# Performance work log

Hardware: AMD Instinct MI355X
Metric: run time of the kernel (lower is better)

Reference implementation:

```python
import jax, jax.numpy as jnp
import numpy as np

B, N_KV, N_Q = 32, 4096, 8
D_INP, D_SLOT, HEADS, MLP_H = 256, 256, 4, 1024
ITERS = 3
EPS = 1e-8


def _ln(x, g, b, eps=1e-5):
    m = jnp.mean(x, axis=-1, keepdims=True)
    v = jnp.var(x, axis=-1, keepdims=True)
    return (x - m) * jax.lax.rsqrt(v + eps) * g + b


def setup_inputs() -> dict:
    key = jax.random.key(0)
    ks = jax.random.split(key, 12)
    def w(k, shape, fan_in):
        return jax.random.normal(k, shape, jnp.float32) / np.float32(np.sqrt(fan_in))
    return {
        "inputs": jax.random.normal(ks[0], (B, N_KV, D_INP), jnp.float32),
        "slots": jax.random.normal(ks[1], (B, N_Q, D_SLOT), jnp.float32),
        "ln_in_g": jnp.ones((D_INP,), jnp.float32), "ln_in_b": jnp.zeros((D_INP,), jnp.float32),
        "ln_slot_g": jnp.ones((D_SLOT,), jnp.float32), "ln_slot_b": jnp.zeros((D_SLOT,), jnp.float32),
        "ln_mlp_g": jnp.ones((D_SLOT,), jnp.float32), "ln_mlp_b": jnp.zeros((D_SLOT,), jnp.float32),
        "Wq": w(ks[2], (D_SLOT, D_SLOT), D_SLOT),
        "Wk": w(ks[3], (D_SLOT, D_INP), D_INP),
        "Wv": w(ks[4], (D_SLOT, D_INP), D_INP),
        "W_ih": w(ks[5], (3 * D_SLOT, D_SLOT), D_SLOT),
        "W_hh": w(ks[6], (3 * D_SLOT, D_SLOT), D_SLOT),
        "b_ih": jnp.zeros((3 * D_SLOT,), jnp.float32),
        "b_hh": jnp.zeros((3 * D_SLOT,), jnp.float32),
        "W1": w(ks[7], (MLP_H, D_SLOT), D_SLOT), "b1": jnp.zeros((MLP_H,), jnp.float32),
        "W2": w(ks[8], (D_SLOT, MLP_H), MLP_H), "b2": jnp.zeros((D_SLOT,), jnp.float32),
    }


def reference(inputs, slots, ln_in_g, ln_in_b, ln_slot_g, ln_slot_b, ln_mlp_g, ln_mlp_b,
              Wq, Wk, Wv, W_ih, W_hh, b_ih, b_hh, W1, b1, W2, b2):
    Bb, Nkv, _ = inputs.shape
    _, Nq, Ds = slots.shape
    hd = Ds // HEADS

    x = _ln(inputs, ln_in_g, ln_in_b)
    # k, v: [B, H, N_kv, hd]; k pre-scaled by hd**-0.5 as in the original
    k = (x @ Wk.T).reshape(Bb, Nkv, HEADS, hd).transpose(0, 2, 1, 3) * (hd ** -0.5)
    v = (x @ Wv.T).reshape(Bb, Nkv, HEADS, hd).transpose(0, 2, 1, 3)

    attn_vis = attn_temp = None
    for it in range(ITERS):
        if it == ITERS - 1:
            slots = jax.lax.stop_gradient(slots)
        slots_prev = slots
        s = _ln(slots, ln_slot_g, ln_slot_b)
        q = (s @ Wq.T).reshape(Bb, Nq, HEADS, hd).transpose(0, 2, 1, 3)  # [B,H,Nq,hd]
        logits = jnp.einsum('bhnd,bhqd->bhnq', k, q)  # [B,H,Nkv,Nq]
        # competing softmax: normalize jointly over (head, slot) per input token
        lt = logits.transpose(0, 2, 1, 3).reshape(Bb, Nkv, HEADS * Nq)
        attn = jax.nn.softmax(lt, axis=-1).reshape(Bb, Nkv, HEADS, Nq).transpose(0, 2, 1, 3)
        attn_vis = attn.sum(axis=1)   # [B, Nkv, Nq]
        attn_temp = attn_vis          # original recomputes the identical softmax; same values
        a = attn + EPS
        a = a / a.sum(axis=-2, keepdims=True)  # renormalize over N_kv
        updates = jnp.einsum('bhnq,bhnd->bhqd', a, v).transpose(0, 2, 1, 3).reshape(Bb, Nq, Ds)
        # GRU cell (torch GRUCell math)
        gx = updates @ W_ih.T + b_ih
        gh = slots_prev @ W_hh.T + b_hh
        xr, xz, xn = jnp.split(gx, 3, axis=-1)
        hr, hz, hn = jnp.split(gh, 3, axis=-1)
        r = jax.nn.sigmoid(xr + hr)
        z = jax.nn.sigmoid(xz + hz)
        n = jnp.tanh(xn + r * hn)
        slots = (1.0 - z) * n + z * slots_prev
        # MLP with residual
        m = _ln(slots, ln_mlp_g, ln_mlp_b)
        slots = slots + (jax.nn.relu(m @ W1.T + b1) @ W2.T + b2)
    return slots, attn_vis, attn_temp
```

## Files before the change

### kernel.cpp

```cpp
#include <hip/hip_runtime.h>
#include <math.h>


#define NKV   4096
#define DD    256
#define HQN   32
#define EPSR  1e-8f

#define WS_V      0
#define WS_A0     262144
#define WS_A1     263168
#define WS_C0     264192
#define WS_C1     265216
#define WS_SLOTA  266240
#define WS_SLOTB  331776
#define WS_WQT    397312
#define WS_QF     462848
#define WS_WPGXH  528384
#define WS_WFT    921600
#define WS_WHHT   1314816
#define WS_W1T    1413120
#define WS_W2T    1544192
#define WS_RS     1675264
#define WS_RM     1806336
#define WS_VPART  1937408

typedef float f32x4 __attribute__((ext_vector_type(4)));
typedef short s16x8 __attribute__((ext_vector_type(8)));
typedef int   v2i   __attribute__((ext_vector_type(2)));

__device__ __forceinline__ unsigned bfr(float f) {
    unsigned u = __float_as_uint(f);
    return (u + 0x7fffu + ((u >> 16) & 1u)) >> 16;
}
__device__ __forceinline__ unsigned pk2(float lo, float hi) {
    return bfr(lo) | (bfr(hi) << 16);
}
__device__ __forceinline__ float bf2f(unsigned short us) {
    return __uint_as_float((unsigned)us << 16);
}
__device__ __forceinline__ float bflo(unsigned u) { return __uint_as_float(u << 16); }
__device__ __forceinline__ float bfhi(unsigned u) { return __uint_as_float(u & 0xffff0000u); }

__device__ __forceinline__ v2i tr_read(unsigned addr) {
    v2i d;
    asm volatile("ds_read_b64_tr_b16 %0, %1" : "=v"(d) : "v"(addr));
    return d;
}
__device__ __forceinline__ s16x8 mk_frag(v2i a, v2i b) {
    union { int i[4]; s16x8 s; } u;
    u.i[0] = a.x; u.i[1] = a.y; u.i[2] = b.x; u.i[3] = b.y;
    return u.s;
}

__global__ __launch_bounds__(256) void k_copy(const float* __restrict__ in,
                                              float* __restrict__ out, int n) {
    int i = blockIdx.x * 256 + threadIdx.x;
    if (i < n) out[i] = in[i];
}

__global__ __launch_bounds__(256) void k_tr(const float* __restrict__ in,
                                            float* __restrict__ out, int R, int C) {
    __shared__ float tile[32][33];
    int bx = blockIdx.x * 32, by = blockIdx.y * 32;
    int x = bx + threadIdx.x;
    for (int k = 0; k < 32; k += 8) {
        int y = by + threadIdx.y + k;
        if (x < C && y < R) tile[threadIdx.y + k][threadIdx.x] = in[(size_t)y * C + x];
    }
    __syncthreads();
    int r = by + threadIdx.x;
    for (int k = 0; k < 32; k += 8) {
        int c = bx + threadIdx.y + k;
        if (c < C && r < R) out[(size_t)c * R + r] = tile[threadIdx.x][threadIdx.y + k];
    }
}

__global__ __launch_bounds__(256) void k_wfold(
    const float* __restrict__ Wih, const float* __restrict__ Wv,
    unsigned* __restrict__ WfT2)
{
    __shared__ float wr[256];
    const int c = blockIdx.x, t = threadIdx.x;
    wr[t] = Wih[(size_t)c * 256 + t];
    __syncthreads();
    const float2* wv2 = (const float2*)Wv;
    #pragma unroll
    for (int pp = 0; pp < 2; ++pp) {
        int P = pp * 256 + t;
        int h = P >> 7, p = P & 127;
        float f0 = 0.f, f1 = 0.f;
        #pragma unroll 8
        for (int d = 0; d < 64; ++d) {
            float a = wr[h * 64 + d];
            float2 v = wv2[(size_t)(h * 64 + d) * 128 + p];
            f0 = fmaf(a, v.x, f0); f1 = fmaf(a, v.y, f1);
        }
        WfT2[(size_t)P * 768 + c] = pk2(f0, f1);
    }
}

__global__ __launch_bounds__(256) void k_trpack(
    const float* __restrict__ in, unsigned* __restrict__ out, int R, int C)
{
    const int c2 = blockIdx.x;
    const int t = threadIdx.x;
    for (int q = 0; q < R / 256; ++q) {
        int r = q * 256 + t;
        out[(size_t)c2 * R + r] = pk2(in[(size_t)r * C + 2 * c2],
                                      in[(size_t)r * C + 2 * c2 + 1]);
    }
}

__global__ __launch_bounds__(256) void k_prep_a(
    const float* __restrict__ slots, const float* __restrict__ g_s, const float* __restrict__ b_s,
    const float* __restrict__ wqt, float* __restrict__ qf_g,
    float* __restrict__ A0_g, float* __restrict__ A1_g)
{
    __shared__ float s_row[256];
    __shared__ float red[8];
    const int t = threadIdx.x;
    const int b = blockIdx.x, qi = blockIdx.y;
    const int lane = t & 63, w = t >> 6;

    if (t < 4) { A0_g[b * 32 + t * 8 + qi] = 0.f; A1_g[b * 32 + t * 8 + qi] = 0.f; }

    float v = slots[((size_t)b * 8 + qi) * 256 + t];
    float s0 = v, s1 = v * v;
    #pragma unroll
    for (int o = 32; o >= 1; o >>= 1) { s0 += __shfl_xor(s0, o, 64); s1 += __shfl_xor(s1, o, 64); }
    if (lane == 0) { red[w] = s0; red[4 + w] = s1; }
    __syncthreads();
    {
        float m = (red[0] + red[1] + red[2] + red[3]) * (1.f / 256.f);
        float q2 = (red[4] + red[5] + red[6] + red[7]) * (1.f / 256.f);
        float rs = rsqrtf(q2 - m * m + 1e-5f);
        s_row[t] = (v - m) * rs * g_s[t] + b_s[t];
    }
    __syncthreads();

    float a = 0.f;
    #pragma unroll 8
    for (int j = 0; j < 256; ++j)
        a = fmaf(s_row[j], wqt[j * 256 + t], a);
    qf_g[((size_t)b * 8 + qi) * 256 + t] = a;
}

__global__ __launch_bounds__(256) void k_prep_b(
    const float* __restrict__ qf_g, const float* __restrict__ Wk,
    const float* __restrict__ g_in, const float* __restrict__ b_in,
    unsigned short* __restrict__ wp_bf, float* __restrict__ c0_g, float* __restrict__ c1_g)
{
    __shared__ float qs[512];
    __shared__ float redc[4096];
    const int t = threadIdx.x;
    const int b = blockIdx.x, h = blockIdx.y;
    const int lane = t & 63, w = t >> 6;
    const float LNS = 0.125f * 1.44269504f;

    #pragma unroll
    for (int rep = 0; rep < 2; ++rep) {
        int idx = rep * 256 + t;
        int qi = idx >> 6, d = idx & 63;
        qs[idx] = qf_g[((size_t)b * 8 + qi) * 256 + h * 64 + d];
    }
    __syncthreads();

    float a2[8];
    #pragma unroll
    for (int qi = 0; qi < 8; ++qi) a2[qi] = 0.f;
    #pragma unroll 4
    for (int d = 0; d < 64; ++d) {
        float wv = Wk[(size_t)(h * 64 + d) * 256 + t];
        #pragma unroll
        for (int qi = 0; qi < 8; ++qi) a2[qi] = fmaf(qs[qi * 64 + d], wv, a2[qi]);
    }
    const float gv = g_in[t], bv = b_in[t];
    #pragma unroll
    for (int qi = 0; qi < 8; ++qi) {
        float kv = LNS * a2[qi];
        float we = kv * gv;
        wp_bf[((size_t)b * HQN + h * 8 + qi) * 256 + t] = (unsigned short)bfr(we);
        redc[qi * 256 + t] = we;
        redc[2048 + qi * 256 + t] = kv * bv;
    }
    __syncthreads();
    #pragma unroll
    for (int rep = 0; rep < 2; ++rep) {
        int r = w * 2 + rep;
        float sv1 = redc[r * 256 + lane] + redc[r * 256 + 64 + lane] +
                    redc[r * 256 + 128 + lane] + redc[r * 256 + 192 + lane];
        float sv0 = redc[2048 + r * 256 + lane] + redc[2048 + r * 256 + 64 + lane] +
                    redc[2048 + r * 256 + 128 + lane] + redc[2048 + r * 256 + 192 + lane];
        #pragma unroll
        for (int o = 32; o >= 1; o >>= 1) {
            sv1 += __shfl_xor(sv1, o, 64);
            sv0 += __shfl_xor(sv0, o, 64);
        }
        if (lane == 0) {
            c1_g[b * 32 + h * 8 + r] = sv1;
            c0_g[b * 32 + h * 8 + r] = sv0;
        }
    }
}

__device__ __forceinline__ void load_x(const float* __restrict__ inp, int b, int n0,
                                       int tok_s, int seg8, float4* ld) {
    const float4* row4 = (const float4*)(inp + ((size_t)b * NKV + n0 + tok_s) * 256);
    #pragma unroll
    for (int u = 0; u < 8; ++u) ld[u] = row4[(u >> 2) * 32 + seg8 * 4 + (u & 3)];
}

__device__ __forceinline__ void pack_x(const float4* ld, char* dst, int tok_s, int seg8) {
    #pragma unroll
    for (int c = 0; c < 2; ++c) {
        int nt = seg8 + 8 * c;
        #pragma unroll
        for (int h = 0; h < 2; ++h) {
            float4 fa = ld[c * 4 + h * 2], fb = ld[c * 4 + h * 2 + 1];
            uint4 pk;
            pk.x = pk2(fa.x, fa.y); pk.y = pk2(fa.z, fa.w);
            pk.z = pk2(fb.x, fb.y); pk.w = pk2(fb.z, fb.w);
            *(uint4*)(dst + nt * 1040 + tok_s * 32 + h * 16) = pk;
        }
    }
}

__device__ __forceinline__ void calc_stats(const float4* ld, float* sb,
                                           float* __restrict__ rs_g, float* __restrict__ rm_g,
                                           int b, int n0, int tok_s, int seg8) {
    float s0 = 0.f, s1 = 0.f;
    #pragma unroll
    for (int u = 0; u < 8; ++u) {
        float4 v = ld[u];
        s0 += v.x + v.y + v.z + v.w;
        s1 = fmaf(v.x, v.x, s1); s1 = fmaf(v.y, v.y, s1);
        s1 = fmaf(v.z, v.z, s1); s1 = fmaf(v.w, v.w, s1);
    }
    s0 += __shfl_xor(s0, 1, 64); s1 += __shfl_xor(s1, 1, 64);
    s0 += __shfl_xor(s0, 2, 64); s1 += __shfl_xor(s1, 2, 64);
    s0 += __shfl_xor(s0, 4, 64); s1 += __shfl_xor(s1, 4, 64);
    float m  = s0 * (1.f / 256.f);
    float rs = rsqrtf(s1 * (1.f / 256.f) - m * m + 1e-5f);
    if (seg8 == 0) {
        sb[tok_s] = rs;
        sb[32 + tok_s] = rs * m;
        rs_g[b * 4096 + n0 + tok_s] = rs;
        rm_g[b * 4096 + n0 + tok_s] = rs * m;
    }
}

template<int STATS, int WVIS>
__global__ __launch_bounds__(256) void k_attn(
    const float* __restrict__ inp, const unsigned short* __restrict__ wp_bf,
    const float* __restrict__ c0_g, const float* __restrict__ c1_g,
    float* __restrict__ vpart, float* __restrict__ A0_g, float* __restrict__ A1_g,
    float* __restrict__ rs_g, float* __restrict__ rm_g,
    float* __restrict__ out_vis, float* __restrict__ out_temp)
{
    __shared__ unsigned short xb[2][8320];
    __shared__ unsigned short wl[8192];
    __shared__ unsigned short pt[1024];
    __shared__ float stats[2][64];
    __shared__ float redm[64];
    __shared__ float reds[64];

    const int t = threadIdx.x;
    const int l = t & 63, w = t >> 6;
    const int g = l >> 4, li = l & 15;
    const int b = blockIdx.y, kb = blockIdx.x;

    char* xbB = (char*)xb;
    char* wlB = (char*)wl;
    char* ptB = (char*)pt;
    const int tok_s = t >> 3, seg8 = t & 7;
    const int cbase = kb * 4;

    {
        const uint4* wp4 = (const uint4*)wp_bf + ((size_t)b * 8192 + (t >> 3) * 256 + (t & 7) * 32) / 8;
        const int hq = t >> 3, sg = t & 7;
        #pragma unroll
        for (int q = 0; q < 4; ++q) {
            uint4 v = wp4[q];
            *(uint4*)(wlB + hq * 512 + (((sg * 4 + q) ^ (hq & 7)) * 16)) = v;
        }
    }

    const int Mt = w & 1, Nt = w >> 1;
    const int hqB = Nt * 16 + li;
    const float c0r = c0_g[b * 32 + hqB];
    const float c1r = c1_g[b * 32 + hqB];
    const int MtV = w >> 1, ntb = (w & 1) * 8;
    const int hqA = MtV * 16 + li;

    f32x4 av[8];
    #pragma unroll
    for (int u = 0; u < 8; ++u) av[u] = (f32x4){0.f, 0.f, 0.f, 0.f};
    float A0acc = 0.f, A1acc = 0.f;

    const unsigned xbase = (unsigned)(uintptr_t)xbB;

    {
        float4 ldA[8];
        load_x(inp, b, cbase * 32, tok_s, seg8, ldA);
        if (STATS) {
            calc_stats(ldA, &stats[0][0], rs_g, rm_g, b, cbase * 32, tok_s, seg8);
        } else {
            if (t < 32) stats[0][t] = rs_g[b * 4096 + cbase * 32 + t];
            else if (t < 64) stats[0][t] = rm_g[b * 4096 + cbase * 32 + t - 32];
        }
        pack_x(ldA, xbB, tok_s, seg8);
    }
    __syncthreads();

    #pragma unroll
    for (int ci = 0; ci < 4; ++ci) {
        const int cur = ci & 1, nxt = cur ^ 1;
        const int n0 = (cbase + ci) * 32;
        char* xc = xbB + cur * 16640;
        char* xn = xbB + nxt * 16640;

        float4 ldN[8];
        if (ci < 3) load_x(inp, b, n0 + 32, tok_s, seg8, ldN);
        __builtin_amdgcn_sched_barrier(0);

        f32x4 accS = (f32x4){0.f, 0.f, 0.f, 0.f};
        #pragma unroll
        for (int kk = 0; kk < 8; ++kk) {
            s16x8 af = *(const s16x8*)(xc + (kk * 2 + (g >> 1)) * 1040 +
                                       (Mt * 16 + li) * 32 + (g & 1) * 16);
            s16x8 bf = *(const s16x8*)(wlB + hqB * 512 + (((kk * 4 + g) ^ (hqB & 7)) * 16));
            accS = __builtin_amdgcn_mfma_f32_16x16x32_bf16(af, bf, accS, 0, 0, 0);
        }

        float lg[4], rsv[4], rmv[4], mh[4], ex[4], aa[4];
        #pragma unroll
        for (int r = 0; r < 4; ++r) {
            int tokr = Mt * 16 + g * 4 + r;
            rsv[r] = stats[cur][tokr];
            rmv[r] = stats[cur][32 + tokr];
            lg[r] = fmaf(rsv[r], accS[r], fmaf(-rmv[r], c1r, c0r));
        }
        #pragma unroll
        for (int r = 0; r < 4; ++r) {
            float v = lg[r];
            v = fmaxf(v, __shfl_xor(v, 1, 64));
            v = fmaxf(v, __shfl_xor(v, 2, 64));
            v = fmaxf(v, __shfl_xor(v, 4, 64));
            v = fmaxf(v, __shfl_xor(v, 8, 64));
            mh[r] = v;
            ex[r] = exp2f(lg[r] - v);
            float s = ex[r];
            s += __shfl_xor(s, 1, 64);
            s += __shfl_xor(s, 2, 64);
            s += __shfl_xor(s, 4, 64);
            s += __shfl_xor(s, 8, 64);
            if (li == 0) {
                int tokr = Mt * 16 + g * 4 + r;
                redm[tokr * 2 + Nt] = v;
                reds[tokr * 2 + Nt] = s;
            }
        }
        __syncthreads();
        #pragma unroll
        for (int r = 0; r < 4; ++r) {
            int tokr = Mt * 16 + g * 4 + r;
            float m0 = redm[tokr * 2], m1 = redm[tokr * 2 + 1];
            float mx = fmaxf(m0, m1);
            float tot = reds[tokr * 2] * exp2f(m0 - mx) + reds[tokr * 2 + 1] * exp2f(m1 - mx);
            aa[r] = ex[r] * (exp2f(mh[r] - mx) / tot);
            A0acc += aa[r];
            A1acc = fmaf(aa[r], rmv[r], A1acc);
        }
        {
            uint2 pw;
            pw.x = pk2(aa[0] * rsv[0], aa[1] * rsv[1]);
            pw.y = pk2(aa[2] * rsv[2], aa[3] * rsv[3]);
            int tokb = Mt * 16 + g * 4;
            int slot = (tokb >> 3) ^ ((hqB >> 1) & 3);
            *(uint2*)(ptB + hqB * 64 + slot * 16 + (tokb & 7) * 2) = pw;
        }
        __syncthreads();

        if (WVIS) {
            int tk = t >> 3, q = t & 7;
            float sv = 0.f;
            #pragma unroll
            for (int h = 0; h < 4; ++h) {
                int hq = h * 8 + q;
                int slot = (tk >> 3) ^ ((hq >> 1) & 3);
                sv += bf2f(*(const unsigned short*)(ptB + hq * 64 + slot * 16 + (tk & 7) * 2));
            }
            float vv = sv / stats[cur][tk];
            size_t o = ((size_t)b * NKV + n0 + tk) * 8 + q;
            out_vis[o] = vv; out_temp[o] = vv;
        }

        if (ci < 3) {
            if (STATS) {
                calc_stats(ldN, &stats[nxt][0], rs_g, rm_g, b, n0 + 32, tok_s, seg8);
            } else {
                if (t < 32) stats[nxt][t] = rs_g[b * 4096 + n0 + 32 + t];
                else if (t < 64) stats[nxt][t] = rm_g[b * 4096 + n0 + 32 + t - 32];
            }
            pack_x(ldN, xn, tok_s, seg8);
        }

        {
            s16x8 pa = *(const s16x8*)(ptB + hqA * 64 + ((g ^ ((hqA >> 1) & 3)) * 16));
            unsigned abase = xbase + cur * 16640 + g * 256 + li * 8;
            v2i t0a = tr_read(abase + (ntb + 0) * 1040);
            v2i t0b = tr_read(abase + (ntb + 0) * 1040 + 128);
            v2i t1a = tr_read(abase + (ntb + 1) * 1040);
            v2i t1b = tr_read(abase + (ntb + 1) * 1040 + 128);
            v2i t2a = tr_read(abase + (ntb + 2) * 1040);
            v2i t2b = tr_read(abase + (ntb + 2) * 1040 + 128);
            v2i t3a = tr_read(abase + (ntb + 3) * 1040);
            v2i t3b = tr_read(abase + (ntb + 3) * 1040 + 128);
            asm volatile("s_waitcnt lgkmcnt(0)" ::: "memory");
            __builtin_amdgcn_sched_barrier(0);
            av[0] = __builtin_amdgcn_mfma_f32_16x16x32_bf16(pa, mk_frag(t0a, t0b), av[0], 0, 0, 0);
            av[1] = __builtin_amdgcn_mfma_f32_16x16x32_bf16(pa, mk_frag(t1a, t1b), av[1], 0, 0, 0);
            av[2] = __builtin_amdgcn_mfma_f32_16x16x32_bf16(pa, mk_frag(t2a, t2b), av[2], 0, 0, 0);
            av[3] = __builtin_amdgcn_mfma_f32_16x16x32_bf16(pa, mk_frag(t3a, t3b), av[3], 0, 0, 0);
            v2i t4a = tr_read(abase + (ntb + 4) * 1040);
            v2i t4b = tr_read(abase + (ntb + 4) * 1040 + 128);
            v2i t5a = tr_read(abase + (ntb + 5) * 1040);
            v2i t5b = tr_read(abase + (ntb + 5) * 1040 + 128);
            v2i t6a = tr_read(abase + (ntb + 6) * 1040);
            v2i t6b = tr_read(abase + (ntb + 6) * 1040 + 128);
            v2i t7a = tr_read(abase + (ntb + 7) * 1040);
            v2i t7b = tr_read(abase + (ntb + 7) * 1040 + 128);
            asm volatile("s_waitcnt lgkmcnt(0)" ::: "memory");
            __builtin_amdgcn_sched_barrier(0);
            av[4] = __builtin_amdgcn_mfma_f32_16x16x32_bf16(pa, mk_frag(t4a, t4b), av[4], 0, 0, 0);
            av[5] = __builtin_amdgcn_mfma_f32_16x16x32_bf16(pa, mk_frag(t5a, t5b), av[5], 0, 0, 0);
            av[6] = __builtin_amdgcn_mfma_f32_16x16x32_bf16(pa, mk_frag(t6a, t6b), av[6], 0, 0, 0);
            av[7] = __builtin_amdgcn_mfma_f32_16x16x32_bf16(pa, mk_frag(t7a, t7b), av[7], 0, 0, 0);
        }
        __syncthreads();
    }

    A0acc += __shfl_xor(A0acc, 16, 64); A0acc += __shfl_xor(A0acc, 32, 64);
    A1acc += __shfl_xor(A1acc, 16, 64); A1acc += __shfl_xor(A1acc, 32, 64);
    if (g == 0) {
        atomicAdd(A0_g + b * 32 + hqB, A0acc);
        atomicAdd(A1_g + b * 32 + hqB, A1acc);
    }
    float* vp = vpart + ((size_t)(b * 32 + kb) * 32) * 256;
    #pragma unroll
    for (int i = 0; i < 8; ++i) {
        int j = (ntb + i) * 16 + li;
        #pragma unroll
        for (int r = 0; r < 4; ++r) {
            int hq = MtV * 16 + g * 4 + r;
            vp[(size_t)hq * 256 + j] = av[i][r];
        }
    }
}

__global__ __launch_bounds__(256) void k_vred(
    const float* __restrict__ vpart, float* __restrict__ V_g)
{
    const int t = threadIdx.x;
    const int b = blockIdx.x, hq = blockIdx.y;
    const float* p = vpart + ((size_t)(b * 32) * 32 + hq) * 256 + t;
    float s = 0.f;
    #pragma unroll 8
    for (int kb = 0; kb < 32; ++kb)
        s += p[(size_t)kb * 8192];
    V_g[((size_t)b * 32 + hq) * 256 + t] = s;
}

__global__ __launch_bounds__(256) void k_gates(
    const float* __restrict__ V_g, const float* __restrict__ A0_g,
    const float* __restrict__ A1_g,
    const float* __restrict__ g_in, const float* __restrict__ b_in,
    const float* __restrict__ slot_cur,
    const unsigned* __restrict__ WfT2, const unsigned* __restrict__ WhhT2,
    float* __restrict__ gxh, float* __restrict__ slot_nxt)
{
    __shared__ __align__(16) float aT[1024 * 4];
    const int t = threadIdx.x;
    const int rg = blockIdx.y;
    const int chunk = blockIdx.x;
    const int row0 = rg * 4;
    float acc0 = 0.f, acc1 = 0.f, acc2 = 0.f, acc3 = 0.f;

    if (chunk == 0) {
        #pragma unroll
        for (int rr = 0; rr < 4; ++rr)
            slot_nxt[(size_t)(row0 + rr) * 256 + t] = 0.f;
    }

    if (chunk < 3) {
        const int b = rg >> 1, qi0 = (rg & 1) * 4;
        const float gt = g_in[t], bt = b_in[t];
        #pragma unroll
        for (int kk = 0; kk < 4; ++kk) {
            float4 y4;
            #pragma unroll
            for (int rr = 0; rr < 4; ++rr) {
                int hq = kk * 8 + qi0 + rr;
                float A0 = A0_g[b * 32 + hq], A1 = A1_g[b * 32 + hq];
                float den = A0 + EPSR * (float)NKV;
                float vv = V_g[((size_t)b * 32 + hq) * 256 + t];
                float yv = (gt * (vv - A1) + bt * A0) / den;
                ((float*)&y4)[rr] = yv;
            }
            *(float4*)(aT + (kk * 256 + t) * 4) = y4;
        }
        __syncthreads();
        const unsigned* wp = WfT2 + chunk * 256 + t;
        #pragma unroll 4
        for (int k2 = 0; k2 < 512; ++k2) {
            unsigned wv = wp[(size_t)k2 * 768];
            float w0 = bflo(wv), w1 = bfhi(wv);
            float4 a0 = *(const float4*)(aT + 8 * k2);
            float4 a1 = *(const float4*)(aT + 8 * k2 + 4);
            acc0 = fmaf(a0.x, w0, acc0); acc0 = fmaf(a1.x, w1, acc0);
            acc1 = fmaf(a0.y, w0, acc1); acc1 = fmaf(a1.y, w1, acc1);
            acc2 = fmaf(a0.z, w0, acc2); acc2 = fmaf(a1.z, w1, acc2);
            acc3 = fmaf(a0.w, w0, acc3); acc3 = fmaf(a1.w, w1, acc3);
        }
        float* go = gxh + (size_t)row0 * 1536 + chunk * 256 + t;
        go[0] = acc0; go[1536] = acc1; go[3072] = acc2; go[4608] = acc3;
    } else {
        const int gc = chunk - 3;
        {
            float4 y4;
            #pragma unroll
            for (int rr = 0; rr < 4; ++rr)
                ((float*)&y4)[rr] = slot_cur[(size_t)(row0 + rr) * 256 + t];
            *(float4*)(aT + t * 4) = y4;
        }
        __syncthreads();
        const unsigned* wp = WhhT2 + gc * 256 + t;
        #pragma unroll 4
        for (int k2 = 0; k2 < 128; ++k2) {
            unsigned wv = wp[(size_t)k2 * 768];
            float w0 = bflo(wv), w1 = bfhi(wv);
            float4 a0 = *(const float4*)(aT + 8 * k2);
            float4 a1 = *(const float4*)(aT + 8 * k2 + 4);
            acc0 = fmaf(a0.x, w0, acc0); acc0 = fmaf(a1.x, w1, acc0);
            acc1 = fmaf(a0.y, w0, acc1); acc1 = fmaf(a1.y, w1, acc1);
            acc2 = fmaf(a0.z, w0, acc2); acc2 = fmaf(a1.z, w1, acc2);
            acc3 = fmaf(a0.w, w0, acc3); acc3 = fmaf(a1.w, w1, acc3);
        }
        float* go = gxh + (size_t)row0 * 1536 + 768 + gc * 256 + t;
        go[0] = acc0; go[1536] = acc1; go[3072] = acc2; go[4608] = acc3;
    }
}

__global__ __launch_bounds__(256) void k_mlp(
    const float* __restrict__ gxh, const float* __restrict__ slot_cur,
    const float* __restrict__ bih, const float* __restrict__ bhh,
    const float* __restrict__ gm, const float* __restrict__ bm,
    const unsigned* __restrict__ W1T2, const float* __restrict__ b1,
    const unsigned* __restrict__ W2T2, const float* __restrict__ b2,
    float* __restrict__ slot_nxt)
{
    __shared__ __align__(16) float mT[1024];
    __shared__ float sm_l[4][256];
    __shared__ float h1_l[4][256];
    __shared__ float lnst[8];
    const int t = threadIdx.x;
    const int rg = blockIdx.y, chunk = blockIdx.x;
    const int row0 = rg * 4;
    const int lane = t & 63, w = t >> 6;

    const float bi0 = bih[t], bi1 = bih[256 + t], bi2 = bih[512 + t];
    const float bh0 = bhh[t], bh1 = bhh[256 + t], bh2 = bhh[512 + t];
    float smid[4];
    #pragma unroll
    for (int rr = 0; rr < 4; ++rr) {
        const float* gr = gxh + (size_t)(row0 + rr) * 1536;
        float gx0 = gr[t], gx1 = gr[256 + t], gx2 = gr[512 + t];
        float gh0 = gr[768 + t], gh1 = gr[1024 + t], gh2 = gr[1280 + t];
        float spv = slot_cur[(size_t)(row0 + rr) * 256 + t];
        float r = 1.f / (1.f + __expf(-(gx0 + bi0 + gh0 + bh0)));
        float z = 1.f / (1.f + __expf(-(gx1 + bi1 + gh1 + bh1)));
        float n = tanhf(gx2 + bi2 + r * (gh2 + bh2));
        smid[rr] = (1.f - z) * n + z * spv;
        sm_l[rr][t] = smid[rr];
    }
    __syncthreads();
    {
        float4 v = *(const float4*)(&sm_l[w][lane * 4]);
        float s0 = v.x + v.y + v.z + v.w;
        float s1 = v.x * v.x + v.y * v.y + v.z * v.z + v.w * v.w;
        #pragma unroll
        for (int o = 32; o >= 1; o >>= 1) { s0 += __shfl_xor(s0, o, 64); s1 += __shfl_xor(s1, o, 64); }
        if (lane == 0) {
            float mu = s0 * (1.f / 256.f);
            lnst[w * 2] = mu;
            lnst[w * 2 + 1] = rsqrtf(s1 * (1.f / 256.f) - mu * mu + 1e-5f);
        }
    }
    __syncthreads();
    {
        const float gmt = gm[t], bmt = bm[t];
        float4 m4;
        #pragma unroll
        for (int rr = 0; rr < 4; ++rr)
            ((float*)&m4)[rr] = (smid[rr] - lnst[rr * 2]) * lnst[rr * 2 + 1] * gmt + bmt;
        *(float4*)(mT + t * 4) = m4;
    }
    __syncthreads();

    {
        float acc0 = 0.f, acc1 = 0.f, acc2 = 0.f, acc3 = 0.f;
        const unsigned* wp = W1T2 + chunk * 256 + t;
        #pragma unroll 4
        for (int k2 = 0; k2 < 128; ++k2) {
            unsigned wv = wp[(size_t)k2 * 1024];
            float w0 = bflo(wv), w1 = bfhi(wv);
            float4 a0 = *(const float4*)(mT + 8 * k2);
            float4 a1 = *(const float4*)(mT + 8 * k2 + 4);
            acc0 = fmaf(a0.x, w0, acc0); acc0 = fmaf(a1.x, w1, acc0);
            acc1 = fmaf(a0.y, w0, acc1); acc1 = fmaf(a1.y, w1, acc1);
            acc2 = fmaf(a0.z, w0, acc2); acc2 = fmaf(a1.z, w1, acc2);
            acc3 = fmaf(a0.w, w0, acc3); acc3 = fmaf(a1.w, w1, acc3);
        }
        const float b1t = b1[chunk * 256 + t];
        h1_l[0][t] = fmaxf(acc0 + b1t, 0.f);
        h1_l[1][t] = fmaxf(acc1 + b1t, 0.f);
        h1_l[2][t] = fmaxf(acc2 + b1t, 0.f);
        h1_l[3][t] = fmaxf(acc3 + b1t, 0.f);
    }
    __syncthreads();

    {
        float o0 = 0.f, o1 = 0.f, o2 = 0.f, o3 = 0.f;
        const unsigned* wp = W2T2 + (size_t)(chunk * 128) * 256 + t;
        #pragma unroll 4
        for (int k2 = 0; k2 < 128; ++k2) {
            unsigned wv = wp[(size_t)k2 * 256];
            float w0 = bflo(wv), w1 = bfhi(wv);
            float a00 = h1_l[0][2 * k2], a01 = h1_l[0][2 * k2 + 1];
            float a10 = h1_l[1][2 * k2], a11 = h1_l[1][2 * k2 + 1];
            float a20 = h1_l[2][2 * k2], a21 = h1_l[2][2 * k2 + 1];
            float a30 = h1_l[3][2 * k2], a31 = h1_l[3][2 * k2 + 1];
            o0 = fmaf(a00, w0, o0); o0 = fmaf(a01, w1, o0);
            o1 = fmaf(a10, w0, o1); o1 = fmaf(a11, w1, o1);
            o2 = fmaf(a20, w0, o2); o2 = fmaf(a21, w1, o2);
            o3 = fmaf(a30, w0, o3); o3 = fmaf(a31, w1, o3);
        }
        const float b2t = b2[t];
        float base0 = (chunk == 0) ? smid[0] + b2t : 0.f;
        float base1 = (chunk == 0) ? smid[1] + b2t : 0.f;
        float base2 = (chunk == 0) ? smid[2] + b2t : 0.f;
        float base3 = (chunk == 0) ? smid[3] + b2t : 0.f;
        atomicAdd(slot_nxt + (size_t)(row0 + 0) * 256 + t, o0 + base0);
        atomicAdd(slot_nxt + (size_t)(row0 + 1) * 256 + t, o1 + base1);
        atomicAdd(slot_nxt + (size_t)(row0 + 2) * 256 + t, o2 + base2);
        atomicAdd(slot_nxt + (size_t)(row0 + 3) * 256 + t, o3 + base3);
    }
}

extern "C" void kernel_launch(void* const* d_in, const int* in_sizes, int n_in,
                              void* d_out, int out_size, void* d_ws, size_t ws_size,
                              hipStream_t stream) {
    const float* inp     = (const float*)d_in[0];
    const float* slots0  = (const float*)d_in[1];
    const float* ln_in_g = (const float*)d_in[2];
    const float* ln_in_b = (const float*)d_in[3];
    const float* ln_s_g  = (const float*)d_in[4];
    const float* ln_s_b  = (const float*)d_in[5];
    const float* ln_m_g  = (const float*)d_in[6];
    const float* ln_m_b  = (const float*)d_in[7];
    const float* Wq  = (const float*)d_in[8];
    const float* Wk  = (const float*)d_in[9];
    const float* Wv  = (const float*)d_in[10];
    const float* Wih = (const float*)d_in[11];
    const float* Whh = (const float*)d_in[12];
    const float* bih = (const float*)d_in[13];
    const float* bhh = (const float*)d_in[14];
    const float* W1  = (const float*)d_in[15];
    const float* b1  = (const float*)d_in[16];
    const float* W2  = (const float*)d_in[17];
    const float* b2  = (const float*)d_in[18];

    float* ws = (float*)d_ws;
    float* V_g   = ws + WS_V;
    float* A0_g  = ws + WS_A0;
    float* A1_g  = ws + WS_A1;
    float* c0_g  = ws + WS_C0;
    float* c1_g  = ws + WS_C1;
    float* slotA = ws + WS_SLOTA;
    float* slotB = ws + WS_SLOTB;
    float* wqt   = ws + WS_WQT;
    float* qf_g  = ws + WS_QF;
    float* gxh   = ws + WS_WPGXH;
    unsigned short* wp_bf = (unsigned short*)(ws + WS_WPGXH);
    unsigned* WfT2  = (unsigned*)(ws + WS_WFT);
    unsigned* WhhT2 = (unsigned*)(ws + WS_WHHT);
    unsigned* W1T2  = (unsigned*)(ws + WS_W1T);
    unsigned* W2T2  = (unsigned*)(ws + WS_W2T);
    float* rs_g  = ws + WS_RS;
    float* rm_g  = ws + WS_RM;
    float* vpart = ws + WS_VPART;

    float* out_slots = (float*)d_out;
    float* out_vis   = out_slots + 32 * 8 * 256;
    float* out_temp  = out_vis + 32 * 4096 * 8;

    k_tr<<<dim3(8, 8), dim3(32, 8), 0, stream>>>(Wq, wqt, 256, 256);
    k_wfold<<<768, 256, 0, stream>>>(Wih, Wv, WfT2);
    k_trpack<<<128, 256, 0, stream>>>(Whh, WhhT2, 768, 256);
    k_trpack<<<128, 256, 0, stream>>>(W1, W1T2, 1024, 256);
    k_trpack<<<512, 256, 0, stream>>>(W2, W2T2, 256, 1024);
    k_copy<<<256, 256, 0, stream>>>(slots0, slotA, 65536);

    for (int it = 0; it < 3; ++it) {
        float* cur = (it & 1) ? slotB : slotA;
        float* nxt = (it & 1) ? slotA : slotB;
        k_prep_a<<<dim3(32, 8), 256, 0, stream>>>(cur, ln_s_g, ln_s_b, wqt, qf_g,
                                                  A0_g, A1_g);
        k_prep_b<<<dim3(32, 4), 256, 0, stream>>>(qf_g, Wk, ln_in_g, ln_in_b,
                                                  wp_bf, c0_g, c1_g);
        if (it == 0)
            k_attn<1, 0><<<dim3(32, 32), 256, 0, stream>>>(
                inp, wp_bf, c0_g, c1_g, vpart, A0_g, A1_g, rs_g, rm_g, out_vis, out_temp);
        else if (it == 1)
            k_attn<0, 0><<<dim3(32, 32), 256, 0, stream>>>(
                inp, wp_bf, c0_g, c1_g, vpart, A0_g, A1_g, rs_g, rm_g, out_vis, out_temp);
        else
            k_attn<0, 1><<<dim3(32, 32), 256, 0, stream>>>(
                inp, wp_bf, c0_g, c1_g, vpart, A0_g, A1_g, rs_g, rm_g, out_vis, out_temp);
        k_vred<<<dim3(32, 32), 256, 0, stream>>>(vpart, V_g);
        k_gates<<<dim3(6, 64), 256, 0, stream>>>(
            V_g, A0_g, A1_g, ln_in_g, ln_in_b, cur, WfT2, WhhT2, gxh, nxt);
        k_mlp<<<dim3(4, 64), 256, 0, stream>>>(
            gxh, cur, bih, bhh, ln_m_g, ln_m_b, W1T2, b1, W2T2, b2, nxt);
    }
    k_copy<<<256, 256, 0, stream>>>(slotB, out_slots, 65536);
}
```

Baseline: 476.3 us.

## Split attention over more blocks and write final slots directly to output

Makes the number of token chunks per attention block a template parameter. When the workspace is large enough, it launches twice as many blocks with two chunks each and has the reduction kernel sum 64 partials instead of 32, which raises occupancy and parallelism at the cost of more partial-sum traffic. It also removes the final copy kernel: on the last iteration the gate and MLP kernels zero and atomically accumulate into the output buffer alongside the slot buffer. The extra atomics double the final-iteration MLP write traffic, and the shorter per-block chunk loop leaves less room to hide the next chunk's loads.

```diff
diff --git a/kernel.cpp b/kernel.cpp
--- a/kernel.cpp
+++ b/kernel.cpp
@@ -250,7 +250,7 @@
     }
 }
 
-template<int STATS, int WVIS>
+template<int NC, int STATS, int WVIS>
 __global__ __launch_bounds__(256) void k_attn(
     const float* __restrict__ inp, const unsigned short* __restrict__ wp_bf,
     const float* __restrict__ c0_g, const float* __restrict__ c1_g,
@@ -258,6 +258,7 @@
     float* __restrict__ rs_g, float* __restrict__ rm_g,
     float* __restrict__ out_vis, float* __restrict__ out_temp)
 {
+    constexpr int KBMAX = 128 / NC;
     __shared__ unsigned short xb[2][8320];
     __shared__ unsigned short wl[8192];
     __shared__ unsigned short pt[1024];
@@ -274,7 +275,7 @@
     char* wlB = (char*)wl;
     char* ptB = (char*)pt;
     const int tok_s = t >> 3, seg8 = t & 7;
-    const int cbase = kb * 4;
+    const int cbase = kb * NC;
 
     {
         const uint4* wp4 = (const uint4*)wp_bf + ((size_t)b * 8192 + (t >> 3) * 256 + (t & 7) * 32) / 8;
@@ -314,14 +315,14 @@
     __syncthreads();
 
     #pragma unroll
-    for (int ci = 0; ci < 4; ++ci) {
+    for (int ci = 0; ci < NC; ++ci) {
         const int cur = ci & 1, nxt = cur ^ 1;
         const int n0 = (cbase + ci) * 32;
         char* xc = xbB + cur * 16640;
         char* xn = xbB + nxt * 16640;
 
         float4 ldN[8];
-        if (ci < 3) load_x(inp, b, n0 + 32, tok_s, seg8, ldN);
+        if (ci < NC - 1) load_x(inp, b, n0 + 32, tok_s, seg8, ldN);
         __builtin_amdgcn_sched_barrier(0);
 
         f32x4 accS = (f32x4){0.f, 0.f, 0.f, 0.f};
@@ -396,7 +397,7 @@
             out_vis[o] = vv; out_temp[o] = vv;
         }
 
-        if (ci < 3) {
+        if (ci < NC - 1) {
             if (STATS) {
                 calc_stats(ldN, &stats[nxt][0], rs_g, rm_g, b, n0 + 32, tok_s, seg8);
             } else {
@@ -447,7 +448,7 @@
         atomicAdd(A0_g + b * 32 + hqB, A0acc);
         atomicAdd(A1_g + b * 32 + hqB, A1acc);
     }
-    float* vp = vpart + ((size_t)(b * 32 + kb) * 32) * 256;
+    float* vp = vpart + ((size_t)(b * KBMAX + kb) * 32) * 256;
     #pragma unroll
     for (int i = 0; i < 8; ++i) {
         int j = (ntb + i) * 16 + li;
@@ -459,15 +460,16 @@
     }
 }
 
+template<int KBMAX>
 __global__ __launch_bounds__(256) void k_vred(
     const float* __restrict__ vpart, float* __restrict__ V_g)
 {
     const int t = threadIdx.x;
     const int b = blockIdx.x, hq = blockIdx.y;
-    const float* p = vpart + ((size_t)(b * 32) * 32 + hq) * 256 + t;
+    const float* p = vpart + ((size_t)(b * KBMAX) * 32 + hq) * 256 + t;
     float s = 0.f;
     #pragma unroll 8
-    for (int kb = 0; kb < 32; ++kb)
+    for (int kb = 0; kb < KBMAX; ++kb)
         s += p[(size_t)kb * 8192];
     V_g[((size_t)b * 32 + hq) * 256 + t] = s;
 }
@@ -478,7 +480,8 @@
     const float* __restrict__ g_in, const float* __restrict__ b_in,
     const float* __restrict__ slot_cur,
     const unsigned* __restrict__ WfT2, const unsigned* __restrict__ WhhT2,
-    float* __restrict__ gxh, float* __restrict__ slot_nxt)
+    float* __restrict__ gxh, float* __restrict__ slot_nxt,
+    float* __restrict__ out_slots)
 {
     __shared__ __align__(16) float aT[1024 * 4];
     const int t = threadIdx.x;
@@ -489,8 +492,10 @@
 
     if (chunk == 0) {
         #pragma unroll
-        for (int rr = 0; rr < 4; ++rr)
+        for (int rr = 0; rr < 4; ++rr) {
             slot_nxt[(size_t)(row0 + rr) * 256 + t] = 0.f;
+            if (out_slots) out_slots[(size_t)(row0 + rr) * 256 + t] = 0.f;
+        }
     }
 
     if (chunk < 3) {
@@ -558,7 +563,7 @@
     const float* __restrict__ gm, const float* __restrict__ bm,
     const unsigned* __restrict__ W1T2, const float* __restrict__ b1,
     const unsigned* __restrict__ W2T2, const float* __restrict__ b2,
-    float* __restrict__ slot_nxt)
+    float* __restrict__ slot_nxt, float* __restrict__ out_slots)
 {
     __shared__ __align__(16) float mT[1024];
     __shared__ float sm_l[4][256];
@@ -647,14 +652,20 @@
             o3 = fmaf(a30, w0, o3); o3 = fmaf(a31, w1, o3);
         }
         const float b2t = b2[t];
-        float base0 = (chunk == 0) ? smid[0] + b2t : 0.f;
-        float base1 = (chunk == 0) ? smid[1] + b2t : 0.f;
-        float base2 = (chunk == 0) ? smid[2] + b2t : 0.f;
-        float base3 = (chunk == 0) ? smid[3] + b2t : 0.f;
-        atomicAdd(slot_nxt + (size_t)(row0 + 0) * 256 + t, o0 + base0);
-        atomicAdd(slot_nxt + (size_t)(row0 + 1) * 256 + t, o1 + base1);
-        atomicAdd(slot_nxt + (size_t)(row0 + 2) * 256 + t, o2 + base2);
-        atomicAdd(slot_nxt + (size_t)(row0 + 3) * 256 + t, o3 + base3);
+        float p0 = o0 + ((chunk == 0) ? smid[0] + b2t : 0.f);
+        float p1 = o1 + ((chunk == 0) ? smid[1] + b2t : 0.f);
+        float p2 = o2 + ((chunk == 0) ? smid[2] + b2t : 0.f);
+        float p3 = o3 + ((chunk == 0) ? smid[3] + b2t : 0.f);
+        atomicAdd(slot_nxt + (size_t)(row0 + 0) * 256 + t, p0);
+        atomicAdd(slot_nxt + (size_t)(row0 + 1) * 256 + t, p1);
+        atomicAdd(slot_nxt + (size_t)(row0 + 2) * 256 + t, p2);
+        atomicAdd(slot_nxt + (size_t)(row0 + 3) * 256 + t, p3);
+        if (out_slots) {
+            atomicAdd(out_slots + (size_t)(row0 + 0) * 256 + t, p0);
+            atomicAdd(out_slots + (size_t)(row0 + 1) * 256 + t, p1);
+            atomicAdd(out_slots + (size_t)(row0 + 2) * 256 + t, p2);
+            atomicAdd(out_slots + (size_t)(row0 + 3) * 256 + t, p3);
+        }
     }
 }
 
@@ -701,6 +712,8 @@
     float* rm_g  = ws + WS_RM;
     float* vpart = ws + WS_VPART;
 
+    const int useNC2 = (ws_size >= (size_t)(WS_VPART + 32ull * 64 * 8192) * 4) ? 1 : 0;
+
     float* out_slots = (float*)d_out;
     float* out_vis   = out_slots + 32 * 8 * 256;
     float* out_temp  = out_vis + 32 * 4096 * 8;
@@ -719,20 +732,34 @@
                                                   A0_g, A1_g);
         k_prep_b<<<dim3(32, 4), 256, 0, stream>>>(qf_g, Wk, ln_in_g, ln_in_b,
                                                   wp_bf, c0_g, c1_g);
-        if (it == 0)
-            k_attn<1, 0><<<dim3(32, 32), 256, 0, stream>>>(
-                inp, wp_bf, c0_g, c1_g, vpart, A0_g, A1_g, rs_g, rm_g, out_vis, out_temp);
-        else if (it == 1)
-            k_attn<0, 0><<<dim3(32, 32), 256, 0, stream>>>(
-                inp, wp_bf, c0_g, c1_g, vpart, A0_g, A1_g, rs_g, rm_g, out_vis, out_temp);
-        else
-            k_attn<0, 1><<<dim3(32, 32), 256, 0, stream>>>(
-                inp, wp_bf, c0_g, c1_g, vpart, A0_g, A1_g, rs_g, rm_g, out_vis, out_temp);
-        k_vred<<<dim3(32, 32), 256, 0, stream>>>(vpart, V_g);
+        if (useNC2) {
+            if (it == 0)
+                k_attn<2, 1, 0><<<dim3(64, 32), 256, 0, stream>>>(
+                    inp, wp_bf, c0_g, c1_g, vpart, A0_g, A1_g, rs_g, rm_g, out_vis, out_temp);
+            else if (it == 1)
+                k_attn<2, 0, 0><<<dim3(64, 32), 256, 0, stream>>>(
+                    inp, wp_bf, c0_g, c1_g, vpart, A0_g, A1_g, rs_g, rm_g, out_vis, out_temp);
+            else
+                k_attn<2, 0, 1><<<dim3(64, 32), 256, 0, stream>>>(
+                    inp, wp_bf, c0_g, c1_g, vpart, A0_g, A1_g, rs_g, rm_g, out_vis, out_temp);
+            k_vred<64><<<dim3(32, 32), 256, 0, stream>>>(vpart, V_g);
+        } else {
+            if (it == 0)
+                k_attn<4, 1, 0><<<dim3(32, 32), 256, 0, stream>>>(
+                    inp, wp_bf, c0_g, c1_g, vpart, A0_g, A1_g, rs_g, rm_g, out_vis, out_temp);
+            else if (it == 1)
+                k_attn<4, 0, 0><<<dim3(32, 32), 256, 0, stream>>>(
+                    inp, wp_bf, c0_g, c1_g, vpart, A0_g, A1_g, rs_g, rm_g, out_vis, out_temp);
+            else
+                k_attn<4, 0, 1><<<dim3(32, 32), 256, 0, stream>>>(
+                    inp, wp_bf, c0_g, c1_g, vpart, A0_g, A1_g, rs_g, rm_g, out_vis, out_temp);
+            k_vred<32><<<dim3(32, 32), 256, 0, stream>>>(vpart, V_g);
+        }
         k_gates<<<dim3(6, 64), 256, 0, stream>>>(
-            V_g, A0_g, A1_g, ln_in_g, ln_in_b, cur, WfT2, WhhT2, gxh, nxt);
+            V_g, A0_g, A1_g, ln_in_g, ln_in_b, cur, WfT2, WhhT2, gxh, nxt,
+            (it == 2) ? out_slots : nullptr);
         k_mlp<<<dim3(4, 64), 256, 0, stream>>>(
-            gxh, cur, bih, bhh, ln_m_g, ln_m_b, W1T2, b1, W2T2, b2, nxt);
-    }
-    k_copy<<<256, 256, 0, stream>>>(slotB, out_slots, 65536);
-}
+            gxh, cur, bih, bhh, ln_m_g, ln_m_b, W1T2, b1, W2T2, b2, nxt,
+            (it == 2) ? out_slots : nullptr);
+    }
+}
```

Measured after the change: 474.3 us. About the same (-0.4%).
